# Kernel optimization log

Measured on AMD Instinct MI355X. Metric: run time of the kernel, lower is better.

The kernel has to match this reference:

```python
import jax, jax.numpy as jnp
import numpy as np

N_NODES = 10000
IN_F = 512
OUT_F = 512
N_EDGES = 160000
GRID_SIZE = 5      # KAN spline grid intervals
SPLINE_ORDER = 3   # cubic B-splines -> GRID_SIZE + SPLINE_ORDER = 8 basis fns per input dim
ALPHA = 0.2        # LeakyReLU negative slope


def _grid():
    # uniform extended grid on [-1, 1], shape [GRID_SIZE + 2*SPLINE_ORDER + 1]
    step = 2.0 / GRID_SIZE
    return jnp.arange(-SPLINE_ORDER, GRID_SIZE + SPLINE_ORDER + 1, dtype=jnp.float32) * step - 1.0


def _b_splines(x, grid):
    # x: [N, in] -> basis: [N, in, GRID_SIZE + SPLINE_ORDER] via Cox-de Boor recursion
    x = x[..., None]  # [N, in, 1]
    bases = ((x >= grid[:-1]) & (x < grid[1:])).astype(x.dtype)  # order-0
    for p in range(1, SPLINE_ORDER + 1):
        left = (x - grid[: -(p + 1)]) / (grid[p:-1] - grid[: -(p + 1)]) * bases[..., :-1]
        right = (grid[p + 1:] - x) / (grid[p + 1:] - grid[1:-p]) * bases[..., 1:]
        bases = left + right
    return bases


def setup_inputs() -> dict:
    key = jax.random.key(0)
    k1, k2, k3, k4, k5, k6 = jax.random.split(key, 6)
    h = jax.random.normal(k1, (N_NODES, IN_F), dtype=jnp.float32)
    edge_index = jax.random.randint(k2, (2, N_EDGES), 0, N_NODES, dtype=jnp.int64)
    xav = float(np.sqrt(2.0 / (IN_F + OUT_F))) * 1.414
    W = jax.random.normal(k3, (IN_F, OUT_F), dtype=jnp.float32) * xav
    a = jax.random.normal(k4, (2 * OUT_F, 1), dtype=jnp.float32) * float(np.sqrt(2.0 / (2 * OUT_F + 1)))
    base_w = jax.random.normal(k5, (OUT_F, IN_F), dtype=jnp.float32) * xav
    n_coef = GRID_SIZE + SPLINE_ORDER
    spline_w = jax.random.normal(k6, (OUT_F, IN_F, n_coef), dtype=jnp.float32) * 0.1
    return {"h": h, "W": W, "a": a, "base_w": base_w, "spline_w": spline_w, "edge_index": edge_index}


def reference(h, W, a, base_w, spline_w, edge_index):
    HW = h @ W  # [N, out]
    row, col = edge_index[0], edge_index[1]
    # a_input @ a == HW_i @ a[:out] + HW_j @ a[out:] (same math, avoids the concat)
    s = HW @ a[:OUT_F, 0]   # [N]
    t = HW @ a[OUT_F:, 0]   # [N]
    e = jax.nn.leaky_relu(s[row] + t[col], negative_slope=ALPHA)  # [E]
    # segment softmax keyed on destination (row)
    m = jax.ops.segment_max(e, row, num_segments=N_NODES)
    ex = jnp.exp(e - m[row])
    den = jax.ops.segment_sum(ex, row, num_segments=N_NODES)
    att = ex / den[row]
    # dropout p=0.6 is identity in eval mode
    # scatter-add aggregation of raw features h[col] (as in the source)
    agg = jax.ops.segment_sum(att[:, None] * h[col], row, num_segments=N_NODES)  # [N, in]
    # KANLayer: silu base path + B-spline path (efficient-KAN formulation)
    grid = _grid()
    basis = _b_splines(agg, grid)  # [N, in, n_coef]
    out = jax.nn.silu(agg) @ base_w.T + jnp.einsum('nip,oip->no', basis, spline_w)
    return out
```

## Files before the change

kernel.cpp:

```cpp
#include <hip/hip_runtime.h>
#include <hip/hip_bf16.h>
#include <math.h>

#define N_NODES 10000
#define IN_F 512
#define OUT_F 512
#define N_EDGES 160000
#define K_SPLINE 4096
#define K_TOTAL 4608
#define NBK 144
#define NBM 628
#define ALPHA 0.2f

typedef __attribute__((ext_vector_type(8))) short short8;
typedef __attribute__((ext_vector_type(4))) float f32x4;
typedef unsigned short ushort_t;
typedef unsigned long long u64;

__device__ __forceinline__ unsigned bfpair(float a, float b) {
    __hip_bfloat162 h2 = __float22bfloat162_rn(make_float2(a, b));
    return *reinterpret_cast<unsigned*>(&h2);
}
__device__ __forceinline__ float bflo(unsigned u) { return __uint_as_float(u << 16); }
__device__ __forceinline__ float bfhi(unsigned u) { return __uint_as_float(u & 0xffff0000u); }

__device__ __forceinline__ float silu_f(float x) {
    return x / (1.f + __expf(-x));
}

__device__ __forceinline__ uint4 spline_window(float x) {
    float xc = (x + 2.2f) * 2.5f;
    float fc = floorf(xc);
    int c = (int)fc;
    float u = xc - fc;
    float omu = 1.f - u;
    float u2 = u * u, u3 = u2 * u;
    float n0 = (1.f / 6.f) * omu * omu * omu;
    float n1 = 0.5f * u3 - u2 + (2.f / 3.f);
    float n2 = -0.5f * u3 + 0.5f * u2 + 0.5f * u + (1.f / 6.f);
    float n3 = (1.f / 6.f) * u3;
    u64 V = (u64)bfpair(n0, n1) | ((u64)bfpair(n2, n3) << 32);
    int sh = (c - 3) * 16;
    u64 lo, hi;
    if (c < 0 || c > 10)    { lo = 0; hi = 0; }
    else if (sh >= 64)      { lo = 0; hi = V << (sh - 64); }
    else if (sh > 0)        { lo = V << sh; hi = V >> (64 - sh); }
    else if (sh == 0)       { lo = V; hi = 0; }
    else                    { lo = V >> (-sh); hi = 0; }
    uint4 pk;
    pk.x = (unsigned)lo; pk.y = (unsigned)(lo >> 32);
    pk.z = (unsigned)hi; pk.w = (unsigned)(hi >> 32);
    return pk;
}

__global__ void fused1_kernel(const float* __restrict__ W, const float* __restrict__ a,
                              float* __restrict__ wa0, float* __restrict__ wa1,
                              const float* __restrict__ base_w, const float* __restrict__ spline_w,
                              ushort_t* __restrict__ Bt,
                              const float* __restrict__ h, ushort_t* __restrict__ hb,
                              const int* __restrict__ ei, int* __restrict__ deg) {
    int b = blockIdx.x;
    int tid = threadIdx.x;
    if (b < 128) {
        int w = tid >> 6, l = tid & 63;
        int i = b * 4 + w;
        float s0 = 0.f, s1 = 0.f;
        #pragma unroll
        for (int oo = 0; oo < 8; ++oo) {
            int o = l + oo * 64;
            float wv = W[(size_t)i * OUT_F + o];
            s0 += wv * a[o];
            s1 += wv * a[OUT_F + o];
        }
        #pragma unroll
        for (int off = 32; off > 0; off >>= 1) {
            s0 += __shfl_down(s0, off, 64);
            s1 += __shfl_down(s1, off, 64);
        }
        if (l == 0) { wa0[i] = s0; wa1[i] = s1; }
    } else if (b < 1280) {
        int gid = (b - 128) * 256 + tid;
        int o = gid / 576;
        int kb8 = gid - o * 576;
        int k0 = kb8 * 8;
        float4 x0, x1;
        if (k0 < K_SPLINE) {
            const float4* p = (const float4*)(spline_w + (size_t)o * K_SPLINE + k0);
            x0 = p[0]; x1 = p[1];
        } else {
            const float4* p = (const float4*)(base_w + (size_t)o * IN_F + (k0 - K_SPLINE));
            x0 = p[0]; x1 = p[1];
        }
        int frag = (k0 >> 5) * 32 + (o >> 4);
        int lane = ((kb8 & 3) << 4) + (o & 15);
        uint4 pk;
        pk.x = bfpair(x0.x, x0.y);
        pk.y = bfpair(x0.z, x0.w);
        pk.z = bfpair(x1.x, x1.y);
        pk.w = bfpair(x1.z, x1.w);
        *(uint4*)(Bt + ((size_t)frag * 64 + lane) * 8) = pk;
    } else if (b < 3780) {
        int id = (b - 1280) * 256 + tid;
        const float4* p = (const float4*)(h + (size_t)id * 8);
        float4 a0 = p[0], a1 = p[1];
        uint4 pk;
        pk.x = bfpair(a0.x, a0.y);
        pk.y = bfpair(a0.z, a0.w);
        pk.z = bfpair(a1.x, a1.y);
        pk.w = bfpair(a1.z, a1.w);
        *(uint4*)(hb + (size_t)id * 8) = pk;
    } else {
        int k = (b - 3780) * 256 + tid;
        if (k < N_EDGES) atomicAdd(&deg[ei[k]], 1);
    }
}

__global__ void fused2_kernel(const float* __restrict__ h, const float* __restrict__ wa0,
                              const float* __restrict__ wa1,
                              float* __restrict__ s, float* __restrict__ t,
                              const int* __restrict__ deg, int* __restrict__ off,
                              int* __restrict__ cursor) {
    __shared__ int sb[256];
    int b = blockIdx.x;
    int tid = threadIdx.x;
    if (b < 2500) {
        int w = tid >> 6, l = tid & 63;
        int n = b * 4 + w;
        const float4* hp = (const float4*)(h + (size_t)n * IN_F);
        float4 hA = hp[l], hB = hp[l + 64];
        float4 wA0 = ((const float4*)wa0)[l], wB0 = ((const float4*)wa0)[l + 64];
        float4 wA1 = ((const float4*)wa1)[l], wB1 = ((const float4*)wa1)[l + 64];
        float ss = hA.x*wA0.x + hA.y*wA0.y + hA.z*wA0.z + hA.w*wA0.w
                 + hB.x*wB0.x + hB.y*wB0.y + hB.z*wB0.z + hB.w*wB0.w;
        float tt = hA.x*wA1.x + hA.y*wA1.y + hA.z*wA1.z + hA.w*wA1.w
                 + hB.x*wB1.x + hB.y*wB1.y + hB.z*wB1.z + hB.w*wB1.w;
        #pragma unroll
        for (int o = 32; o > 0; o >>= 1) {
            ss += __shfl_down(ss, o, 64);
            tt += __shfl_down(tt, o, 64);
        }
        if (l == 0) { s[n] = ss; t[n] = tt; }
    } else {
        int d[40];
        int tot = 0;
        #pragma unroll
        for (int j = 0; j < 40; ++j) {
            int idx = tid * 40 + j;
            d[j] = (idx < N_NODES) ? deg[idx] : 0;
            tot += d[j];
        }
        sb[tid] = tot;
        __syncthreads();
        for (int sd = 1; sd < 256; sd <<= 1) {
            int v = (tid >= sd) ? sb[tid - sd] : 0;
            __syncthreads();
            sb[tid] += v;
            __syncthreads();
        }
        int run = (tid > 0) ? sb[tid - 1] : 0;
        #pragma unroll
        for (int j = 0; j < 40; ++j) {
            int idx = tid * 40 + j;
            if (idx < N_NODES) { off[idx] = run; cursor[idx] = run; }
            run += d[j];
        }
        if (tid == 255) off[N_NODES] = sb[255];
    }
}

__global__ void fill_kernel(const int* __restrict__ ei, int* __restrict__ cursor,
                            int* __restrict__ csr_col) {
    int k = blockIdx.x * 256 + threadIdx.x;
    if (k < N_EDGES) {
        int r = ei[k];
        int c = ei[N_EDGES + k];
        int p = atomicAdd(&cursor[r], 1);
        csr_col[p] = c;
    }
}

__global__ __launch_bounds__(256) void agg_kernel(
    const ushort_t* __restrict__ hb, const float* __restrict__ s,
    const float* __restrict__ t, const int* __restrict__ off,
    const int* __restrict__ csr, float* __restrict__ agg) {
    int w = threadIdx.x >> 6, l = threadIdx.x & 63;
    int n = blockIdx.x * 4 + w;
    int e0 = off[n], e1 = off[n + 1];
    float sn = s[n];

    float m = -1e30f, den = 0.f;
    for (int k = e0 + l; k < e1; k += 64) {
        float v = sn + t[csr[k]];
        v = (v >= 0.f) ? v : ALPHA * v;
        float mn = fmaxf(m, v);
        den = den * __expf(m - mn) + __expf(v - mn);
        m = mn;
    }
    #pragma unroll
    for (int o = 1; o < 64; o <<= 1) {
        float m2 = __shfl_xor(m, o, 64);
        float d2 = __shfl_xor(den, o, 64);
        float mn = fmaxf(m, m2);
        den = den * __expf(m - mn) + d2 * __expf(m2 - mn);
        m = mn;
    }
    float inv = (den > 0.f) ? 1.f / den : 0.f;

    int hl = l >> 5;
    int lo = l & 31;
    float acc[16];
    #pragma unroll
    for (int i = 0; i < 16; ++i) acc[i] = 0.f;
    const ushort_t* hbl = hb + lo * 16;

    for (int base = e0; base < e1; base += 64) {
        int cnt = e1 - base; if (cnt > 64) cnt = 64;
        int c = 0; float att = 0.f;
        if (l < cnt) {
            c = csr[base + l];
            float v = sn + t[c];
            v = (v >= 0.f) ? v : ALPHA * v;
            att = __expf(v - m) * inv;
        }
        int npair = (cnt + 1) >> 1;
        #pragma unroll 2
        for (int j = 0; j < npair; ++j) {
            int e = 2 * j + hl;
            float aj = __shfl(att, e, 64);
            int cj = __shfl(c, e, 64);
            const ushort_t* rp = hbl + (size_t)cj * IN_F;
            uint4 u0 = *(const uint4*)rp;
            uint4 u1 = *(const uint4*)(rp + 8);
            acc[0]  = fmaf(aj, bflo(u0.x), acc[0]);
            acc[1]  = fmaf(aj, bfhi(u0.x), acc[1]);
            acc[2]  = fmaf(aj, bflo(u0.y), acc[2]);
            acc[3]  = fmaf(aj, bfhi(u0.y), acc[3]);
            acc[4]  = fmaf(aj, bflo(u0.z), acc[4]);
            acc[5]  = fmaf(aj, bfhi(u0.z), acc[5]);
            acc[6]  = fmaf(aj, bflo(u0.w), acc[6]);
            acc[7]  = fmaf(aj, bfhi(u0.w), acc[7]);
            acc[8]  = fmaf(aj, bflo(u1.x), acc[8]);
            acc[9]  = fmaf(aj, bfhi(u1.x), acc[9]);
            acc[10] = fmaf(aj, bflo(u1.y), acc[10]);
            acc[11] = fmaf(aj, bfhi(u1.y), acc[11]);
            acc[12] = fmaf(aj, bflo(u1.z), acc[12]);
            acc[13] = fmaf(aj, bfhi(u1.z), acc[13]);
            acc[14] = fmaf(aj, bflo(u1.w), acc[14]);
            acc[15] = fmaf(aj, bfhi(u1.w), acc[15]);
        }
    }
    #pragma unroll
    for (int i = 0; i < 16; ++i) acc[i] += __shfl_xor(acc[i], 32, 64);

    if (hl == 0) {
        float* arow = agg + (size_t)n * IN_F + lo * 16;
        *(float4*)(arow)      = make_float4(acc[0],  acc[1],  acc[2],  acc[3]);
        *(float4*)(arow + 4)  = make_float4(acc[4],  acc[5],  acc[6],  acc[7]);
        *(float4*)(arow + 8)  = make_float4(acc[8],  acc[9],  acc[10], acc[11]);
        *(float4*)(arow + 12) = make_float4(acc[12], acc[13], acc[14], acc[15]);
    }
}

__global__ __launch_bounds__(256) void expand_kernel(const float* __restrict__ agg,
                                                     ushort_t* __restrict__ Xf) {
    __shared__ float AL[16][516];
    int nb = blockIdx.x;
    int tid = threadIdx.x;

    #pragma unroll
    for (int i = 0; i < 8; ++i) {
        int idx = i * 256 + tid;
        int r = idx >> 7, c4 = idx & 127;
        int n = nb * 16 + r;
        float4 v = (n < N_NODES) ? ((const float4*)(agg + (size_t)n * IN_F))[c4]
                                 : make_float4(0.f, 0.f, 0.f, 0.f);
        *(float4*)&AL[r][c4 * 4] = v;
    }
    __syncthreads();

    int w = tid >> 6, l = tid & 63;
    bool live = (nb * 16 + (l & 15)) < N_NODES;
    #pragma unroll 1
    for (int i = 0; i < 36; ++i) {
        int kb = w + 4 * i;
        uint4 pk = make_uint4(0u, 0u, 0u, 0u);
        if (live) {
            if (kb < 128) {
                int dim = kb * 4 + (l >> 4);
                pk = spline_window(AL[l & 15][dim]);
            } else {
                const float* ap = &AL[l & 15][(kb - 128) * 32 + (l >> 4) * 8];
                float4 x0 = *(const float4*)ap;
                float4 x1 = *(const float4*)(ap + 4);
                pk.x = bfpair(silu_f(x0.x), silu_f(x0.y));
                pk.y = bfpair(silu_f(x0.z), silu_f(x0.w));
                pk.z = bfpair(silu_f(x1.x), silu_f(x1.y));
                pk.w = bfpair(silu_f(x1.z), silu_f(x1.w));
            }
        }
        *(uint4*)(Xf + ((size_t)(nb * NBK + kb) * 64 + l) * 8) = pk;
    }
}

__global__ __launch_bounds__(256, 3) void kan_gemm2(
    const ushort_t* __restrict__ Xf, const ushort_t* __restrict__ Bt,
    float* __restrict__ out) {
    __shared__ ushort_t A_lds[2][4][4][64][8];

    int d = blockIdx.x;
    int g = d >> 5, r = d & 31;
    int bm = g * 8 + (r & 7), bn = r >> 3;
    if (bm >= 157) return;
    int tid = threadIdx.x, w = tid >> 6, l = tid & 63;
    int wc16 = bn * 8 + w * 2;

    f32x4 acc[4][2];
    #pragma unroll
    for (int m = 0; m < 4; ++m)
        #pragma unroll
        for (int nf = 0; nf < 2; ++nf)
            acc[m][nf] = (f32x4){0.f, 0.f, 0.f, 0.f};

    short8 b0[8], b1[8];

    auto stage = [&](int j, int pb) {
        #pragma unroll
        for (int ks = 0; ks < 4; ++ks) {
            const ushort_t* src = Xf + (((size_t)(bm * 4 + w) * NBK + 4 * j + ks) * 64 + l) * 8;
            __builtin_amdgcn_global_load_lds(
                (const __attribute__((address_space(1))) unsigned int*)src,
                (__attribute__((address_space(3))) unsigned int*)&A_lds[pb][ks][w][0][0],
                16, 0, 0);
        }
    };
    auto loadB = [&](int j, short8 (&b)[8]) {
        #pragma unroll
        for (int ks = 0; ks < 4; ++ks) {
            int kb = 4 * j + ks;
            b[ks * 2 + 0] = *(const short8*)(Bt + ((size_t)(kb * 32 + wc16)     * 64 + l) * 8);
            b[ks * 2 + 1] = *(const short8*)(Bt + ((size_t)(kb * 32 + wc16 + 1) * 64 + l) * 8);
        }
    };
    auto compute = [&](int pb, short8 (&b)[8]) {
        #pragma unroll
        for (int ks = 0; ks < 4; ++ks)
            #pragma unroll
            for (int m = 0; m < 4; ++m) {
                short8 af = *(const short8*)&A_lds[pb][ks][m][l][0];
                acc[m][0] = __builtin_amdgcn_mfma_f32_16x16x32_bf16(af, b[ks * 2 + 0], acc[m][0], 0, 0, 0);
                acc[m][1] = __builtin_amdgcn_mfma_f32_16x16x32_bf16(af, b[ks * 2 + 1], acc[m][1], 0, 0, 0);
            }
    };

    stage(0, 0);
    loadB(0, b0);
    __syncthreads();
    for (int j = 0; j < 36; j += 2) {
        if (j + 1 < 36) { stage(j + 1, 1); loadB(j + 1, b1); }
        compute(0, b0);
        __syncthreads();
        if (j + 2 < 36) { stage(j + 2, 0); loadB(j + 2, b0); }
        compute(1, b1);
        __syncthreads();
    }

    #pragma unroll
    for (int m = 0; m < 4; ++m) {
        int r0 = bm * 64 + m * 16 + ((l >> 4) << 2);
        #pragma unroll
        for (int nf = 0; nf < 2; ++nf) {
            int colg = bn * 128 + w * 32 + nf * 16 + (l & 15);
            #pragma unroll
            for (int jr = 0; jr < 4; ++jr) {
                int rr = r0 + jr;
                if (rr < N_NODES) out[(size_t)rr * OUT_F + colg] = acc[m][nf][jr];
            }
        }
    }
}

extern "C" void kernel_launch(void* const* d_in, const int* in_sizes, int n_in,
                              void* d_out, int out_size, void* d_ws, size_t ws_size,
                              hipStream_t stream) {
    const float* h        = (const float*)d_in[0];
    const float* W        = (const float*)d_in[1];
    const float* a        = (const float*)d_in[2];
    const float* base_w   = (const float*)d_in[3];
    const float* spline_w = (const float*)d_in[4];
    const int*   ei       = (const int*)d_in[5];
    float* out = (float*)d_out;

    char* ws = (char*)d_ws;
    size_t cur = 0;
    auto alloc = [&](size_t bytes) -> void* {
        void* p = ws + cur;
        cur += (bytes + 255) & ~(size_t)255;
        return p;
    };
    float* wa0    = (float*)alloc(512 * 4);
    float* wa1    = (float*)alloc(512 * 4);
    float* s      = (float*)alloc(N_NODES * 4);
    float* t      = (float*)alloc(N_NODES * 4);
    int*   deg    = (int*)alloc(N_NODES * 4);
    int*   offp   = (int*)alloc((N_NODES + 1) * 4);
    int*   cursor = (int*)alloc(N_NODES * 4);
    int*   csr    = (int*)alloc(N_EDGES * 4);
    float* agg    = (float*)alloc((size_t)N_NODES * IN_F * 4);
    ushort_t* Bt  = (ushort_t*)alloc((size_t)K_TOTAL * OUT_F * 2);
    ushort_t* hb  = (ushort_t*)alloc((size_t)N_NODES * IN_F * 2);
    ushort_t* Xf  = (ushort_t*)alloc((size_t)NBM * NBK * 64 * 16);
    if (cur > ws_size) return;

    hipMemsetAsync(deg, 0, N_NODES * 4, stream);
    fused1_kernel<<<4405, 256, 0, stream>>>(W, a, wa0, wa1, base_w, spline_w, Bt, h, hb, ei, deg);
    fused2_kernel<<<2501, 256, 0, stream>>>(h, wa0, wa1, s, t, deg, offp, cursor);
    fill_kernel<<<(N_EDGES + 255) / 256, 256, 0, stream>>>(ei, cursor, csr);
    agg_kernel<<<2500, 256, 0, stream>>>(hb, s, t, offp, csr, agg);
    expand_kernel<<<628, 256, 0, stream>>>(agg, Xf);
    kan_gemm2<<<640, 256, 0, stream>>>(Xf, Bt, out);
}
```

Before: 163.8 us.

## Fuse h bf16 conversion with s/t projection and move deg zeroing into kernel

Restructures the preprocessing launches. Zeroing of the degree array now happens inside a small kernel that also computes W·a, which replaces the memset. The h-to-bf16 conversion is merged with the s/t dot products so h is read once instead of twice. The scan then runs as a separate single-block kernel, so the launch count stays the same while one full pass over h (about 20MB) is removed.

```diff
diff --git a/kernel.cpp b/kernel.cpp
--- a/kernel.cpp
+++ b/kernel.cpp
@@ -53,12 +53,9 @@
     return pk;
 }
 
-__global__ void fused1_kernel(const float* __restrict__ W, const float* __restrict__ a,
+__global__ void wa_deg_kernel(const float* __restrict__ W, const float* __restrict__ a,
                               float* __restrict__ wa0, float* __restrict__ wa1,
-                              const float* __restrict__ base_w, const float* __restrict__ spline_w,
-                              ushort_t* __restrict__ Bt,
-                              const float* __restrict__ h, ushort_t* __restrict__ hb,
-                              const int* __restrict__ ei, int* __restrict__ deg) {
+                              int* __restrict__ deg) {
     int b = blockIdx.x;
     int tid = threadIdx.x;
     if (b < 128) {
@@ -78,8 +75,52 @@
             s1 += __shfl_down(s1, off, 64);
         }
         if (l == 0) { wa0[i] = s0; wa1[i] = s1; }
-    } else if (b < 1280) {
-        int gid = (b - 128) * 256 + tid;
+    } else {
+        int idx = (b - 128) * 256 + tid;
+        if (idx < N_NODES) deg[idx] = 0;
+    }
+}
+
+__global__ void fused1_kernel(const float* __restrict__ h, ushort_t* __restrict__ hb,
+                              const float* __restrict__ wa0, const float* __restrict__ wa1,
+                              float* __restrict__ s, float* __restrict__ t,
+                              const float* __restrict__ base_w, const float* __restrict__ spline_w,
+                              ushort_t* __restrict__ Bt,
+                              const int* __restrict__ ei, int* __restrict__ deg) {
+    int b = blockIdx.x;
+    int tid = threadIdx.x;
+    if (b < 625) {
+        int k = b * 256 + tid;
+        if (k < N_EDGES) atomicAdd(&deg[ei[k]], 1);
+    } else if (b < 3125) {
+        int bb = b - 625;
+        int w = tid >> 6, l = tid & 63;
+        int n = bb * 4 + w;
+        const float* hp = h + (size_t)n * IN_F + l * 8;
+        float4 x0 = *(const float4*)hp;
+        float4 x1 = *(const float4*)(hp + 4);
+        uint4 pk;
+        pk.x = bfpair(x0.x, x0.y);
+        pk.y = bfpair(x0.z, x0.w);
+        pk.z = bfpair(x1.x, x1.y);
+        pk.w = bfpair(x1.z, x1.w);
+        *(uint4*)(hb + (size_t)n * IN_F + l * 8) = pk;
+        const float4* w0 = (const float4*)(wa0 + l * 8);
+        const float4* w1 = (const float4*)(wa1 + l * 8);
+        float4 a0 = w0[0], a1 = w0[1];
+        float4 b0 = w1[0], b1 = w1[1];
+        float ss = x0.x*a0.x + x0.y*a0.y + x0.z*a0.z + x0.w*a0.w
+                 + x1.x*a1.x + x1.y*a1.y + x1.z*a1.z + x1.w*a1.w;
+        float tt = x0.x*b0.x + x0.y*b0.y + x0.z*b0.z + x0.w*b0.w
+                 + x1.x*b1.x + x1.y*b1.y + x1.z*b1.z + x1.w*b1.w;
+        #pragma unroll
+        for (int o = 32; o > 0; o >>= 1) {
+            ss += __shfl_down(ss, o, 64);
+            tt += __shfl_down(tt, o, 64);
+        }
+        if (l == 0) { s[n] = ss; t[n] = tt; }
+    } else {
+        int gid = (b - 3125) * 256 + tid;
         int o = gid / 576;
         int kb8 = gid - o * 576;
         int k0 = kb8 * 8;
@@ -99,73 +140,37 @@
         pk.z = bfpair(x1.x, x1.y);
         pk.w = bfpair(x1.z, x1.w);
         *(uint4*)(Bt + ((size_t)frag * 64 + lane) * 8) = pk;
-    } else if (b < 3780) {
-        int id = (b - 1280) * 256 + tid;
-        const float4* p = (const float4*)(h + (size_t)id * 8);
-        float4 a0 = p[0], a1 = p[1];
-        uint4 pk;
-        pk.x = bfpair(a0.x, a0.y);
-        pk.y = bfpair(a0.z, a0.w);
-        pk.z = bfpair(a1.x, a1.y);
-        pk.w = bfpair(a1.z, a1.w);
-        *(uint4*)(hb + (size_t)id * 8) = pk;
-    } else {
-        int k = (b - 3780) * 256 + tid;
-        if (k < N_EDGES) atomicAdd(&deg[ei[k]], 1);
-    }
-}
-
-__global__ void fused2_kernel(const float* __restrict__ h, const float* __restrict__ wa0,
-                              const float* __restrict__ wa1,
-                              float* __restrict__ s, float* __restrict__ t,
-                              const int* __restrict__ deg, int* __restrict__ off,
-                              int* __restrict__ cursor) {
+    }
+}
+
+__global__ void scan_kernel(const int* __restrict__ deg, int* __restrict__ off,
+                            int* __restrict__ cursor) {
     __shared__ int sb[256];
-    int b = blockIdx.x;
     int tid = threadIdx.x;
-    if (b < 2500) {
-        int w = tid >> 6, l = tid & 63;
-        int n = b * 4 + w;
-        const float4* hp = (const float4*)(h + (size_t)n * IN_F);
-        float4 hA = hp[l], hB = hp[l + 64];
-        float4 wA0 = ((const float4*)wa0)[l], wB0 = ((const float4*)wa0)[l + 64];
-        float4 wA1 = ((const float4*)wa1)[l], wB1 = ((const float4*)wa1)[l + 64];
-        float ss = hA.x*wA0.x + hA.y*wA0.y + hA.z*wA0.z + hA.w*wA0.w
-                 + hB.x*wB0.x + hB.y*wB0.y + hB.z*wB0.z + hB.w*wB0.w;
-        float tt = hA.x*wA1.x + hA.y*wA1.y + hA.z*wA1.z + hA.w*wA1.w
-                 + hB.x*wB1.x + hB.y*wB1.y + hB.z*wB1.z + hB.w*wB1.w;
-        #pragma unroll
-        for (int o = 32; o > 0; o >>= 1) {
-            ss += __shfl_down(ss, o, 64);
-            tt += __shfl_down(tt, o, 64);
-        }
-        if (l == 0) { s[n] = ss; t[n] = tt; }
-    } else {
-        int d[40];
-        int tot = 0;
-        #pragma unroll
-        for (int j = 0; j < 40; ++j) {
-            int idx = tid * 40 + j;
-            d[j] = (idx < N_NODES) ? deg[idx] : 0;
-            tot += d[j];
-        }
-        sb[tid] = tot;
+    int d[40];
+    int tot = 0;
+    #pragma unroll
+    for (int j = 0; j < 40; ++j) {
+        int idx = tid * 40 + j;
+        d[j] = (idx < N_NODES) ? deg[idx] : 0;
+        tot += d[j];
+    }
+    sb[tid] = tot;
+    __syncthreads();
+    for (int sd = 1; sd < 256; sd <<= 1) {
+        int v = (tid >= sd) ? sb[tid - sd] : 0;
         __syncthreads();
-        for (int sd = 1; sd < 256; sd <<= 1) {
-            int v = (tid >= sd) ? sb[tid - sd] : 0;
-            __syncthreads();
-            sb[tid] += v;
-            __syncthreads();
-        }
-        int run = (tid > 0) ? sb[tid - 1] : 0;
-        #pragma unroll
-        for (int j = 0; j < 40; ++j) {
-            int idx = tid * 40 + j;
-            if (idx < N_NODES) { off[idx] = run; cursor[idx] = run; }
-            run += d[j];
-        }
-        if (tid == 255) off[N_NODES] = sb[255];
-    }
+        sb[tid] += v;
+        __syncthreads();
+    }
+    int run = (tid > 0) ? sb[tid - 1] : 0;
+    #pragma unroll
+    for (int j = 0; j < 40; ++j) {
+        int idx = tid * 40 + j;
+        if (idx < N_NODES) { off[idx] = run; cursor[idx] = run; }
+        run += d[j];
+    }
+    if (tid == 255) off[N_NODES] = sb[255];
 }
 
 __global__ void fill_kernel(const int* __restrict__ ei, int* __restrict__ cursor,
@@ -411,10 +416,10 @@
     ushort_t* Xf  = (ushort_t*)alloc((size_t)NBM * NBK * 64 * 16);
     if (cur > ws_size) return;
 
-    hipMemsetAsync(deg, 0, N_NODES * 4, stream);
-    fused1_kernel<<<4405, 256, 0, stream>>>(W, a, wa0, wa1, base_w, spline_w, Bt, h, hb, ei, deg);
-    fused2_kernel<<<2501, 256, 0, stream>>>(h, wa0, wa1, s, t, deg, offp, cursor);
-    fill_kernel<<<(N_EDGES + 255) / 256, 256, 0, stream>>>(ei, cursor, csr);
+    wa_deg_kernel<<<168, 256, 0, stream>>>(W, a, wa0, wa1, deg);
+    fused1_kernel<<<4277, 256, 0, stream>>>(h, hb, wa0, wa1, s, t, base_w, spline_w, Bt, ei, deg);
+    scan_kernel<<<1, 256, 0, stream>>>(deg, offp, cursor);
+    fill_kernel<<<625, 256, 0, stream>>>(ei, cursor, csr);
     agg_kernel<<<2500, 256, 0, stream>>>(hb, s, t, offp, csr, agg);
     expand_kernel<<<628, 256, 0, stream>>>(agg, Xf);
     kan_gemm2<<<640, 256, 0, stream>>>(Xf, Bt, out);
```

Measured after the change: 161.1 us (median of 3 runs). No clear change (-1.6%).
